# Kernel optimization log

Hardware: AMD Instinct MI355X
Metric: run time of the kernel (lower is better)

## Reference

```python
import jax, jax.numpy as jnp
import numpy as np

B, N, C_IN, G = 8, 65536, 16, 64
CH = [16, 16]
EPS = 1e-3  # keras BatchNormalization default epsilon
OFFSETS = [(dx, dy, dz) for dx in (-1, 0, 1) for dy in (-1, 0, 1) for dz in (-1, 0, 1)]
G3 = G * G * G


def setup_inputs() -> dict:
    key = jax.random.key(0)
    k = jax.random.split(key, 8)
    voxel_features = jax.random.normal(k[0], (B, N, C_IN), dtype=jnp.float32)
    # unique active voxel coordinates per example (submanifold sites)
    lin = jax.vmap(lambda kk: jax.random.permutation(kk, G3)[:N])(jax.random.split(k[1], B))
    xyz = jnp.stack([lin // (G * G), (lin // G) % G, lin % G], axis=-1).astype(jnp.int32)
    num_valid_voxels = jax.random.randint(k[2], (B,), N // 2, N + 1).astype(jnp.int32)
    w0 = jax.random.uniform(k[3], (3, 3, 3, C_IN, CH[0]), minval=-0.05, maxval=0.05, dtype=jnp.float32)
    w1 = jax.random.uniform(k[4], (3, 3, 3, CH[0], CH[1]), minval=-0.05, maxval=0.05, dtype=jnp.float32)
    nw0 = jax.random.uniform(k[5], (3, 3, 3, 1, 1), minval=-0.05, maxval=0.05, dtype=jnp.float32)
    nw1 = jax.random.uniform(k[6], (3, 3, 3, 1, 1), minval=-0.05, maxval=0.05, dtype=jnp.float32)
    gamma0 = jnp.ones((CH[0],), jnp.float32); beta0 = jnp.zeros((CH[0],), jnp.float32)
    gamma1 = jnp.ones((CH[1],), jnp.float32); beta1 = jnp.zeros((CH[1],), jnp.float32)
    return dict(voxel_features=voxel_features, voxel_xyz_indices=xyz,
                num_valid_voxels=num_valid_voxels, w0=w0, w1=w1, nw0=nw0, nw1=nw1,
                gamma0=gamma0, beta0=beta0, gamma1=gamma1, beta1=beta1)


def build_neighbor_idx(coords, valid_mask):
    """For each voxel and each 3x3x3 offset, the row index of the active neighbor, or -1."""
    lin = coords[..., 0] * (G * G) + coords[..., 1] * G + coords[..., 2]  # [B,N]
    # invalid (padded) voxels write to a spare slot so they never match as neighbors
    write_lin = jnp.where(valid_mask, lin, G3 + 1)
    idx_map = jnp.full((B, G3 + 2), -1, jnp.int32)
    idx_map = idx_map.at[jnp.arange(B)[:, None], write_lin].set(
        jnp.broadcast_to(jnp.arange(N, dtype=jnp.int32)[None, :], (B, N)))
    brow = jnp.arange(B)[:, None]
    nb = []
    for dx, dy, dz in OFFSETS:
        nx = coords[..., 0] + dx; ny = coords[..., 1] + dy; nz = coords[..., 2] + dz
        inb = (nx >= 0) & (nx < G) & (ny >= 0) & (ny < G) & (nz >= 0) & (nz < G)
        nlin = jnp.where(inb, nx * (G * G) + ny * G + nz, G3)  # slot G3 always -1
        nb.append(idx_map[brow, nlin])
    return jnp.stack(nb, axis=1)  # [B,27,N]


def sparse_conv(feats, nb_idx, valid_mask, w):
    """Submanifold sparse 3D conv: output only at active sites, gathering active neighbors."""
    wf = w.reshape(27, w.shape[3], w.shape[4])  # offsets enumerate kernel taps in order
    out = jnp.zeros((feats.shape[0], feats.shape[1], w.shape[4]), feats.dtype)
    for o in range(27):
        idx = nb_idx[:, o]  # [B,N]
        g = jnp.take_along_axis(feats, jnp.maximum(idx, 0)[..., None], axis=1)
        g = jnp.where((idx >= 0)[..., None], g, 0.0)
        out = out + jnp.einsum('bnc,co->bno', g, wf[o])
    return out * valid_mask[..., None]


def masked_bn(x, valid_mask, num_valid, gamma, beta):
    m = valid_mask[..., None].astype(x.dtype)
    cnt = jnp.sum(num_valid).astype(x.dtype)
    mean = jnp.sum(x * m, axis=(0, 1)) / cnt
    var = jnp.sum(m * jnp.square(x - mean), axis=(0, 1)) / cnt
    xn = (x - mean) * jax.lax.rsqrt(var + EPS) * gamma + beta
    return xn * m  # padded rows are zero-padded, as in the TF layer


def reference(voxel_features, voxel_xyz_indices, num_valid_voxels,
              w0, w1, nw0, nw1, gamma0, beta0, gamma1, beta1):
    valid_mask = jnp.arange(N)[None, :] < num_valid_voxels[:, None]  # [B,N]
    nb_idx = build_neighbor_idx(voxel_xyz_indices, valid_mask)
    ones = jnp.ones((B, N, 1), jnp.float32)
    net = voxel_features
    for w, nw, g, b in ((w0, nw0, gamma0, beta0), (w1, nw1, gamma1, beta1)):
        net = sparse_conv(net, nb_idx, valid_mask, w)
        net_norm = sparse_conv(ones, nb_idx, valid_mask, nw)
        net = net / (1.0 + jnp.abs(net_norm))
        net = masked_bn(net, valid_mask, num_valid_voxels, g, b)
        net = jax.nn.relu(net)
    return net
```

## Files before the change

### kernel.cpp

```cpp
#include <hip/hip_runtime.h>
#include <cstdint>
#include <cstddef>

#define NB 8
#define NN 65536
#define NS (NN + 16)
#define GG 64
#define GG3 (GG*GG*GG)
#define NW (GG3/32)
#define NBLKC 1536
#define EPSC 1e-3f

typedef __bf16 bf16x8 __attribute__((ext_vector_type(8)));
typedef float  f32x4  __attribute__((ext_vector_type(4)));

__device__ __forceinline__ unsigned short f2bf(float f) {
    unsigned u = __builtin_bit_cast(unsigned, f);
    unsigned r = (u + 0x7fffu + ((u >> 16) & 1u)) >> 16;
    return (unsigned short)r;
}
__device__ __forceinline__ unsigned pk2(float a, float b) {
    return (unsigned)f2bf(a) | ((unsigned)f2bf(b) << 16);
}
__device__ __forceinline__ float bf2f(unsigned short s) {
    return __builtin_bit_cast(float, (unsigned)s << 16);
}

__device__ __forceinline__ int site_rank2(const int2* __restrict__ mwb, int lin) {
    int2 mw = mwb[lin >> 5];
    uint32_t w = (uint32_t)mw.x;
    uint32_t bit = 1u << (lin & 31);
    if (!(w & bit)) return -1;
    return mw.y + __popc(w & (bit - 1u));
}

__global__ __launch_bounds__(256) void build_mask_kernel(
    const int* __restrict__ xyz, const int* __restrict__ nvv,
    uint32_t* __restrict__ mask, int* __restrict__ linb,
    const float* __restrict__ w0, const float* __restrict__ w1,
    unsigned short* __restrict__ wf)
{
    int b = blockIdx.y;
    int n = blockIdx.x * 256 + threadIdx.x;
    if (n < nvv[b]) {
        const int* cp = xyz + ((size_t)b * NN + n) * 3;
        int lin = cp[0] * (GG * GG) + cp[1] * GG + cp[2];
        linb[(size_t)b * NN + n] = lin;
        atomicOr(&mask[b * NW + (lin >> 5)], 1u << (lin & 31));
    }
    if (blockIdx.x == 0 && b < 2) {
        const float* w = b ? w1 : w0;
        unsigned short* o = wf + b * 14 * 512;
        for (int idx = threadIdx.x; idx < 14 * 512; idx += 256) {
            int i = idx >> 9;
            int rem = idx & 511;
            int L = rem >> 3, j = rem & 7;
            int quad = L >> 4, nn = L & 15;
            int off = 2 * i + (quad >> 1);
            int c = ((quad & 1) << 3) + j;
            float v = (off < 27) ? w[(off * 16 + c) * 16 + nn] : 0.f;
            o[idx] = f2bf(v);
        }
    }
}

__global__ __launch_bounds__(256) void scan_mask_kernel(
    const uint32_t* __restrict__ mask, int2* __restrict__ mwb)
{
    int b = blockIdx.x;
    const uint32_t* mb = mask + (size_t)b * NW;
    int2* wb = mwb + (size_t)b * NW;
    int t = threadIdx.x;

    uint32_t wv[32];
    int cnts[32];
    int local = 0;
    #pragma unroll
    for (int i = 0; i < 32; i++) {
        wv[i] = mb[t * 32 + i];
        cnts[i] = __popc(wv[i]);
        local += cnts[i];
    }

    __shared__ int sc[256];
    sc[t] = local;
    __syncthreads();
    for (int off = 1; off < 256; off <<= 1) {
        int v = (t >= off) ? sc[t - off] : 0;
        __syncthreads();
        sc[t] += v;
        __syncthreads();
    }
    int base = sc[t] - local;
    #pragma unroll
    for (int i = 0; i < 32; i++) {
        wb[t * 32 + i] = make_int2((int)wv[i], base);
        base += cnts[i];
    }
}

__global__ __launch_bounds__(256) void perm_gather_kernel(
    const int* __restrict__ linb, const int* __restrict__ nvv,
    const int2* __restrict__ mwb,
    const float* __restrict__ feats,
    int2* __restrict__ srow,
    unsigned short* __restrict__ sfeats)
{
    int b = blockIdx.y;
    int n = blockIdx.x * 256 + threadIdx.x;
    int cnt = nvv[b];
    unsigned short* sfb = sfeats + (size_t)b * NS * 16;
    if (blockIdx.x == 0 && threadIdx.x < 16)
        sfb[(size_t)NN * 16 + threadIdx.x] = 0;
    if (n < cnt) {
        int lin = linb[(size_t)b * NN + n];
        int r = site_rank2(mwb + (size_t)b * NW, lin);
        srow[(size_t)b * NN + r] = make_int2(lin, n);
        const float4* fp = (const float4*)(feats + ((size_t)b * NN + n) * 16);
        float4 f0 = fp[0], f1 = fp[1], f2 = fp[2], f3 = fp[3];
        uint4 lo = make_uint4(pk2(f0.x, f0.y), pk2(f0.z, f0.w),
                              pk2(f1.x, f1.y), pk2(f1.z, f1.w));
        uint4 hi = make_uint4(pk2(f2.x, f2.y), pk2(f2.z, f2.w),
                              pk2(f3.x, f3.y), pk2(f3.z, f3.w));
        *(uint4*)(sfb + (size_t)r * 16)     = lo;
        *(uint4*)(sfb + (size_t)r * 16 + 8) = hi;
    }
}

__global__ __launch_bounds__(256, 4) void conv_mfma_kernel(
    const unsigned short* __restrict__ sfeats,
    const int2*     __restrict__ srow,
    const int*      __restrict__ nvv,
    const int2*     __restrict__ mwb,
    const unsigned short* __restrict__ wfrag,
    const float*    __restrict__ nw,
    unsigned short* __restrict__ outbuf,
    float*          __restrict__ stats)
{
    int lane = threadIdx.x & 63;
    int wv = threadIdx.x >> 6;
    int m = lane & 15, quad = lane >> 4;
    int v = lane & 31, h = lane >> 5;
    int wid = blockIdx.x * 4 + wv;

    __shared__ int   jj[4][32][29];
    __shared__ float obuf[4][32][17];
    __shared__ float rrl[4][32];
    __shared__ float red[4][32];
    __shared__ float lnw[27];

    if (threadIdx.x < 27) lnw[threadIdx.x] = nw[threadIdx.x];

    int cnts[8], cum[9];
    cum[0] = 0;
    #pragma unroll
    for (int b = 0; b < 8; b++) {
        cnts[b] = nvv[b];
        cum[b + 1] = cum[b] + ((cnts[b] + 31) >> 5);
    }
    int total = cum[8];

    bf16x8 bfr[14];
    #pragma unroll
    for (int i = 0; i < 14; i++)
        bfr[i] = *(const bf16x8*)(wfrag + i * 512 + lane * 8);
    __syncthreads();

    float psum = 0.f, psq = 0.f;
    int coff = (quad & 1) << 3;

    for (int vp = wid; vp < total; vp += 4 * NBLKC) {
        int b = 0;
        #pragma unroll
        for (int k = 1; k < 8; k++) b += (vp >= cum[k]);
        int r0 = (vp - cum[b]) << 5;
        int cnt = cnts[b];

        const int2* mb = mwb + (size_t)b * NW;
        const unsigned short* fb = sfeats + (size_t)b * NS * 16;
        const int2* sr = srow + (size_t)b * NN;

        int Rv = r0 + v;
        bool vld = Rv < cnt;
        int lin = vld ? sr[Rv].x : 0;
        int x = lin >> 12, y = (lin >> 6) & 63, z = lin & 63;
        int zb = z & 31;
        float nc = 0.f;
        #pragma unroll
        for (int t = 0; t < 5; t++) {
            int c = 2 * t + h;
            bool cok = c < 9;
            int cc = cok ? c : 0;
            int dx = cc / 3 - 1, dy = cc % 3 - 1;
            int nx = x + dx, ny = y + dy;
            bool colok = cok & ((unsigned)nx < 64u) & ((unsigned)ny < 64u);
            int wdi = colok ? (((nx << 12) + (ny << 6) + z) >> 5) : 0;

            int2 mw = make_int2(0, 0);
            if (vld & colok) mw = mb[wdi];
            bool need2 = vld & colok & (((zb == 0) & (z > 0)) | ((zb == 31) & (z < 63)));
            int w2 = wdi + ((zb == 0) ? -1 : 1);
            int2 mw2 = make_int2(0, 0);
            if (need2) mw2 = mb[w2];

            #pragma unroll
            for (int dz = -1; dz <= 1; dz++) {
                int zz = z + dz;
                bool zok = (unsigned)zz < 64u;
                bool same = (dz == 0) | ((dz < 0) ? (zb != 0) : (zb != 31));
                int2 word = same ? mw : mw2;
                int bb = zz & 31;
                uint32_t wm = (uint32_t)word.x;
                bool hit = vld & colok & zok & ((wm >> bb) & 1u);
                int rnk = word.y + __popc(wm & ((1u << bb) - 1u));
                int off = cc * 3 + dz + 1;
                int jv = hit ? rnk : NN;
                if (cok) {
                    jj[wv][v][off] = jv;
                    nc += hit ? lnw[off] : 0.f;
                }
            }
        }
        nc += __shfl_xor(nc, 32, 64);
        if (lane < 32) rrl[wv][v] = 1.f / (1.f + fabsf(nc));

        f32x4 acc0 = {0.f, 0.f, 0.f, 0.f};
        f32x4 acc1 = {0.f, 0.f, 0.f, 0.f};
        #pragma unroll
        for (int i = 0; i < 14; i++) {
            int off = 2 * i + (quad >> 1);
            int idx = off < 27 ? off : 28;
            int j0 = jj[wv][m][idx];      j0 = (off < 27) ? j0 : NN;
            int j1 = jj[wv][m + 16][idx]; j1 = (off < 27) ? j1 : NN;
            bf16x8 a0 = *(const bf16x8*)(fb + (size_t)j0 * 16 + coff);
            bf16x8 a1 = *(const bf16x8*)(fb + (size_t)j1 * 16 + coff);
            acc0 = __builtin_amdgcn_mfma_f32_16x16x32_bf16(a0, bfr[i], acc0, 0, 0, 0);
            acc1 = __builtin_amdgcn_mfma_f32_16x16x32_bf16(a1, bfr[i], acc1, 0, 0, 0);
        }

        #pragma unroll
        for (int hh = 0; hh < 2; hh++) {
            #pragma unroll
            for (int r4 = 0; r4 < 4; r4++) {
                int row = (hh << 4) + (quad << 2) + r4;
                float tval = (hh ? acc1[r4] : acc0[r4]) * rrl[wv][row];
                psum += tval; psq += tval * tval;
                obuf[wv][row][m] = tval;
            }
        }
        {
            int Rr = r0 + v;
            if (Rr < cnt) {
                const float* src = &obuf[wv][v][h * 8];
                uint4 val = make_uint4(pk2(src[0], src[1]), pk2(src[2], src[3]),
                                       pk2(src[4], src[5]), pk2(src[6], src[7]));
                *(uint4*)(outbuf + ((size_t)b * NS + Rr) * 16 + h * 8) = val;
            }
        }
    }

    psum += __shfl_xor(psum, 16, 64); psum += __shfl_xor(psum, 32, 64);
    psq  += __shfl_xor(psq, 16, 64);  psq  += __shfl_xor(psq, 32, 64);
    if (lane < 16) { red[wv][lane] = psum; red[wv][16 + lane] = psq; }
    __syncthreads();
    if (threadIdx.x < 32) {
        float vv = red[0][threadIdx.x] + red[1][threadIdx.x] +
                   red[2][threadIdx.x] + red[3][threadIdx.x];
        atomicAdd(&stats[(blockIdx.x & 15) * 32 + threadIdx.x], vv);
    }
}

__device__ __forceinline__ void compute_sb(
    const float* __restrict__ stats, const int* __restrict__ nvv,
    const float* __restrict__ gamma, const float* __restrict__ beta,
    float* sbs , float* sums )
{
    int tid = threadIdx.x;
    if (tid < 32) {
        float v = 0.f;
        #pragma unroll
        for (int s = 0; s < 16; s++) v += stats[s * 32 + tid];
        sums[tid] = v;
    }
    __syncthreads();
    if (tid < 16) {
        float cnt = 0.f;
        #pragma unroll
        for (int b = 0; b < NB; b++) cnt += (float)nvv[b];
        float mean = sums[tid] / cnt;
        float var  = fmaxf(sums[16 + tid] / cnt - mean * mean, 0.f);
        float scv = gamma[tid] * rsqrtf(var + EPSC);
        sbs[tid]      = scv;
        sbs[16 + tid] = beta[tid] - mean * scv;
    }
    __syncthreads();
}

__global__ __launch_bounds__(256) void bnrelu_sorted_kernel(
    unsigned short* __restrict__ buf, const float* __restrict__ stats,
    const int* __restrict__ nvv,
    const float* __restrict__ gamma, const float* __restrict__ beta)
{
    __shared__ float sbs[32];
    __shared__ float sums[32];
    compute_sb(stats, nvv, gamma, beta, sbs, sums);

    int b = blockIdx.y;
    int r = blockIdx.x * 256 + threadIdx.x;
    if (r > NN) return;
    int cnt = nvv[b];
    unsigned short* op = buf + ((size_t)b * NS + r) * 16;
    if (r < cnt) {
        uint4 xl = *(const uint4*)op, xh = *(const uint4*)(op + 8);
        float y[16];
        #pragma unroll
        for (int c = 0; c < 16; c++) {
            unsigned u = (c < 8) ? ((const unsigned*)&xl)[c >> 1]
                                 : ((const unsigned*)&xh)[(c - 8) >> 1];
            unsigned short sv = (c & 1) ? (unsigned short)(u >> 16)
                                        : (unsigned short)(u & 0xffff);
            y[c] = fmaxf(fmaf(bf2f(sv), sbs[c], sbs[16 + c]), 0.f);
        }
        *(uint4*)op       = make_uint4(pk2(y[0], y[1]), pk2(y[2], y[3]),
                                       pk2(y[4], y[5]), pk2(y[6], y[7]));
        *(uint4*)(op + 8) = make_uint4(pk2(y[8], y[9]), pk2(y[10], y[11]),
                                       pk2(y[12], y[13]), pk2(y[14], y[15]));
    } else if (r == NN) {
        uint4 z = make_uint4(0, 0, 0, 0);
        *(uint4*)op       = z;
        *(uint4*)(op + 8) = z;
    }
}

__global__ __launch_bounds__(256) void final_scatter_kernel(
    const unsigned short* __restrict__ in,
    const int2* __restrict__ srow,
    const float* __restrict__ stats, const int* __restrict__ nvv,
    const float* __restrict__ gamma, const float* __restrict__ beta,
    float* __restrict__ out)
{
    __shared__ float sbs[32];
    __shared__ float sums[32];
    compute_sb(stats, nvv, gamma, beta, sbs, sums);

    int b = blockIdx.y;
    int r = blockIdx.x * 256 + threadIdx.x;
    int cnt = nvv[b];
    if (r < cnt) {
        const uint4* ip = (const uint4*)(in + ((size_t)b * NS + r) * 16);
        uint4 xl = ip[0], xh = ip[1];
        float y[16];
        #pragma unroll
        for (int c = 0; c < 16; c++) {
            unsigned u = (c < 8) ? ((const unsigned*)&xl)[c >> 1]
                                 : ((const unsigned*)&xh)[(c - 8) >> 1];
            unsigned short sv = (c & 1) ? (unsigned short)(u >> 16)
                                        : (unsigned short)(u & 0xffff);
            y[c] = fmaxf(fmaf(bf2f(sv), sbs[c], sbs[16 + c]), 0.f);
        }
        int n = srow[(size_t)b * NN + r].y;
        float4* op = (float4*)(out + ((size_t)b * NN + n) * 16);
        op[0] = make_float4(y[0],  y[1],  y[2],  y[3]);
        op[1] = make_float4(y[4],  y[5],  y[6],  y[7]);
        op[2] = make_float4(y[8],  y[9],  y[10], y[11]);
        op[3] = make_float4(y[12], y[13], y[14], y[15]);
    } else {
        float4 z = make_float4(0.f, 0.f, 0.f, 0.f);
        float4* op = (float4*)(out + ((size_t)b * NN + r) * 16);
        op[0] = z; op[1] = z; op[2] = z; op[3] = z;
    }
}

extern "C" void kernel_launch(void* const* d_in, const int* in_sizes, int n_in,
                              void* d_out, int out_size, void* d_ws, size_t ws_size,
                              hipStream_t stream)
{
    const float* feats  = (const float*)d_in[0];
    const int*   xyz    = (const int*)d_in[1];
    const int*   nvv    = (const int*)d_in[2];
    const float* w0     = (const float*)d_in[3];
    const float* w1     = (const float*)d_in[4];
    const float* nw0    = (const float*)d_in[5];
    const float* nw1    = (const float*)d_in[6];
    const float* gamma0 = (const float*)d_in[7];
    const float* beta0  = (const float*)d_in[8];
    const float* gamma1 = (const float*)d_in[9];
    const float* beta1  = (const float*)d_in[10];
    float* out = (float*)d_out;

    char* ws = (char*)d_ws;
    uint32_t* mask    = (uint32_t*)ws;       ws += (size_t)NB * NW * 4;
    float*    stats1  = (float*)ws;          ws += 16 * 32 * 4;
    float*    stats2  = (float*)ws;          ws += 16 * 32 * 4;
    int2*     mwb     = (int2*)ws;           ws += (size_t)NB * NW * 8;
    int2*     srow    = (int2*)ws;           ws += (size_t)NB * NN * 8;
    int*      linb    = (int*)ws;            ws += (size_t)NB * NN * 4;
    unsigned short* sfA = (unsigned short*)ws; ws += (size_t)NB * NS * 16 * 2;
    unsigned short* sfB = (unsigned short*)ws; ws += (size_t)NB * NS * 16 * 2;
    unsigned short* wfr = (unsigned short*)ws; ws += (size_t)2 * 14 * 512 * 2;

    hipMemsetAsync(mask, 0, (size_t)NB * NW * 4 + 16 * 32 * 4 * 2, stream);

    dim3 gridBN(NN / 256, NB);
    build_mask_kernel<<<gridBN, 256, 0, stream>>>(xyz, nvv, mask, linb, w0, w1, wfr);
    scan_mask_kernel<<<NB, 256, 0, stream>>>(mask, mwb);
    perm_gather_kernel<<<gridBN, 256, 0, stream>>>(linb, nvv, mwb, feats, srow, sfA);

    conv_mfma_kernel<<<NBLKC, 256, 0, stream>>>(
        sfA, srow, nvv, mwb, wfr, nw0, sfB, stats1);
    bnrelu_sorted_kernel<<<dim3(NN / 256 + 1, NB), 256, 0, stream>>>(
        sfB, stats1, nvv, gamma0, beta0);

    conv_mfma_kernel<<<NBLKC, 256, 0, stream>>>(
        sfB, srow, nvv, mwb, wfr + 14 * 512, nw1, sfA, stats2);

    final_scatter_kernel<<<dim3(NN / 256, NB), 256, 0, stream>>>(
        sfA, srow, stats2, nvv, gamma1, beta1, out);
}
```

Before: 256.8 us.

## Raise conv kernel occupancy by aliasing LDS buffers and simplifying the tile loop

The conv kernel's `__launch_bounds__` minimum blocks per CU goes from 4 to 8, and the grid grows from 1536 to 2048 blocks. The per-wave neighbor-index buffer and output staging buffer now share one LDS array, which cuts LDS use so more blocks fit on a CU. The prefix-sum mapping from tiles to batches is replaced by a fixed 2048-tiles-per-batch layout that skips tiles past the valid count. The tighter register budget (about 64 VGPRs per lane) may cause spills, because the 14 weight fragments alone are held in registers, and fixed tiling leaves some waves idle.

Measured after the change: 378.4 us. 47.3% more time.

```diff
diff --git a/kernel.cpp b/kernel.cpp
--- a/kernel.cpp
+++ b/kernel.cpp
@@ -8,7 +8,8 @@
 #define GG 64
 #define GG3 (GG*GG*GG)
 #define NW (GG3/32)
-#define NBLKC 1536
+#define NBLKC 2048
+#define NP32 (NB * 2048)
 #define EPSC 1e-3f
 
 typedef __bf16 bf16x8 __attribute__((ext_vector_type(8)));
@@ -127,7 +128,7 @@
     }
 }
 
-__global__ __launch_bounds__(256, 4) void conv_mfma_kernel(
+__global__ __launch_bounds__(256, 8) void conv_mfma_kernel(
     const unsigned short* __restrict__ sfeats,
     const int2*     __restrict__ srow,
     const int*      __restrict__ nvv,
@@ -143,22 +144,14 @@
     int v = lane & 31, h = lane >> 5;
     int wid = blockIdx.x * 4 + wv;
 
-    __shared__ int   jj[4][32][29];
-    __shared__ float obuf[4][32][17];
+    __shared__ int   ubuf[4][32 * 29];
     __shared__ float rrl[4][32];
     __shared__ float red[4][32];
     __shared__ float lnw[27];
+    int*   jj   = ubuf[wv];
+    float* obuf = (float*)ubuf[wv];
 
     if (threadIdx.x < 27) lnw[threadIdx.x] = nw[threadIdx.x];
-
-    int cnts[8], cum[9];
-    cum[0] = 0;
-    #pragma unroll
-    for (int b = 0; b < 8; b++) {
-        cnts[b] = nvv[b];
-        cum[b + 1] = cum[b] + ((cnts[b] + 31) >> 5);
-    }
-    int total = cum[8];
 
     bf16x8 bfr[14];
     #pragma unroll
@@ -169,12 +162,11 @@
     float psum = 0.f, psq = 0.f;
     int coff = (quad & 1) << 3;
 
-    for (int vp = wid; vp < total; vp += 4 * NBLKC) {
-        int b = 0;
-        #pragma unroll
-        for (int k = 1; k < 8; k++) b += (vp >= cum[k]);
-        int r0 = (vp - cum[b]) << 5;
-        int cnt = cnts[b];
+    for (int pb = wid; pb < NP32; pb += 4 * NBLKC) {
+        int b = pb >> 11;
+        int r0 = (pb & 2047) << 5;
+        int cnt = nvv[b];
+        if (r0 >= cnt) continue;
 
         const int2* mb = mwb + (size_t)b * NW;
         const unsigned short* fb = sfeats + (size_t)b * NS * 16;
@@ -216,7 +208,7 @@
                 int off = cc * 3 + dz + 1;
                 int jv = hit ? rnk : NN;
                 if (cok) {
-                    jj[wv][v][off] = jv;
+                    jj[v * 29 + off] = jv;
                     nc += hit ? lnw[off] : 0.f;
                 }
             }
@@ -230,8 +222,8 @@
         for (int i = 0; i < 14; i++) {
             int off = 2 * i + (quad >> 1);
             int idx = off < 27 ? off : 28;
-            int j0 = jj[wv][m][idx];      j0 = (off < 27) ? j0 : NN;
-            int j1 = jj[wv][m + 16][idx]; j1 = (off < 27) ? j1 : NN;
+            int j0 = jj[m * 29 + idx];        j0 = (off < 27) ? j0 : NN;
+            int j1 = jj[(m + 16) * 29 + idx]; j1 = (off < 27) ? j1 : NN;
             bf16x8 a0 = *(const bf16x8*)(fb + (size_t)j0 * 16 + coff);
             bf16x8 a1 = *(const bf16x8*)(fb + (size_t)j1 * 16 + coff);
             acc0 = __builtin_amdgcn_mfma_f32_16x16x32_bf16(a0, bfr[i], acc0, 0, 0, 0);
@@ -245,13 +237,13 @@
                 int row = (hh << 4) + (quad << 2) + r4;
                 float tval = (hh ? acc1[r4] : acc0[r4]) * rrl[wv][row];
                 psum += tval; psq += tval * tval;
-                obuf[wv][row][m] = tval;
+                obuf[row * 17 + m] = tval;
             }
         }
         {
             int Rr = r0 + v;
             if (Rr < cnt) {
-                const float* src = &obuf[wv][v][h * 8];
+                const float* src = &obuf[v * 17 + h * 8];
                 uint4 val = make_uint4(pk2(src[0], src[1]), pk2(src[2], src[3]),
                                        pk2(src[4], src[5]), pk2(src[6], src[7]));
                 *(uint4*)(outbuf + ((size_t)b * NS + Rr) * 16 + h * 8) = val;
```
